# Kernel tuning notes

Measured on AMD Instinct MI355X. Metric: run time of the kernel, lower is better.

## Reference

```python
import jax, jax.numpy as jnp
import numpy as np

# FlowNetC correlation config (kernel_size=1 -> pointwise patch; pad == max_displacement)
PAD = 20
MAX_DISP = 20
STRIDE2 = 2


def setup_inputs() -> dict:
    key = jax.random.key(0)
    k1, k2 = jax.random.split(key)
    B, C, H, W = 4, 256, 96, 96
    input1 = jax.random.normal(k1, (B, C, H, W), dtype=jnp.float32)
    input2 = jax.random.normal(k2, (B, C, H, W), dtype=jnp.float32)
    return {"input1": input1, "input2": input2}


def _correlation(x1, x2):
    # x1, x2: [B, C, H, W]. Output: [B, D*D, H, W] with D = 2*MAX_DISP//STRIDE2 + 1.
    B, C, H, W = x1.shape
    x2p = jnp.pad(x2, ((0, 0), (0, 0), (PAD, PAD), (PAD, PAD)))
    D = 2 * MAX_DISP // STRIDE2 + 1  # 21
    # start index into padded map = PAD + (disp) where disp = off - MAX_DISP;
    # since PAD == MAX_DISP, start index == off.
    offs = jnp.arange(D, dtype=jnp.int32) * STRIDE2
    dyv, dxv = jnp.meshgrid(offs, offs, indexing="ij")
    pairs = jnp.stack([dyv.ravel(), dxv.ravel()], axis=1)  # [D*D, 2]
    inv_c = jnp.float32(1.0 / C)  # CUDA kernel divides by kernel^2 * C (kernel=1)

    def body(_, p):
        dy, dx = p[0], p[1]
        sl = jax.lax.dynamic_slice(x2p, (0, 0, dy, dx), (B, C, H, W))
        return None, jnp.einsum("bchw,bchw->bhw", x1, sl) * inv_c

    _, corr = jax.lax.scan(body, None, pairs)  # [D*D, B, H, W]
    return corr.transpose(1, 0, 2, 3)  # [B, D*D, H, W]


def reference(input1, input2):
    return _correlation(input1, input2)
```

## Files before the change

kernel.cpp:

```cpp
#include <hip/hip_runtime.h>
#include <hip/hip_bf16.h>


typedef __bf16 bf16x8 __attribute__((ext_vector_type(8)));
typedef float f32x4 __attribute__((ext_vector_type(4)));

#define B_ 4
#define C_ 256
#define H_ 96
#define W_ 96
#define NOFF 21
#define ROWS 96
#define IMG_ELEMS (ROWS * C_)
#define HALF_ELEMS (48 * C_)
#define X1T_ELEMS (B_ * H_ * IMG_ELEMS)

__device__ __forceinline__ unsigned short f32_to_bf16_rne(float f) {
    union { float f; unsigned u; } v; v.f = f;
    unsigned u = v.u;
    return (unsigned short)((u + 0x7fffu + ((u >> 16) & 1u)) >> 16);
}

__device__ __forceinline__ void gl2lds16(const void* g, void* l) {
    __builtin_amdgcn_global_load_lds(
        (const __attribute__((address_space(1))) void*)g,
        (__attribute__((address_space(3))) void*)l, 16, 0, 0);
}

__global__ __launch_bounds__(256) void prep_kernel(const float* __restrict__ x1,
                                                   const float* __restrict__ x2,
                                                   unsigned short* __restrict__ ws) {
    __shared__ float tile[96 * 65];
    int bid = blockIdx.x;
    int cblk  = bid & 3;
    int which = (bid >> 2) & 1;
    int bh    = bid >> 3;
    int h = bh % H_;
    int b = bh / H_;
    int c0 = cblk << 6;

    const float* src = (which ? x2 : x1) + ((size_t)(b * C_ + c0) * H_ + h) * W_;
    unsigned short* dst = ws + (size_t)which * X1T_ELEMS + (size_t)(b * H_ + h) * IMG_ELEMS;

    for (int idx = threadIdx.x; idx < 64 * 96; idx += 256) {
        int c = idx / 96, w = idx - c * 96;
        tile[w * 65 + c] = src[c * (H_ * W_) + w];
    }
    __syncthreads();

    for (int idx = threadIdx.x; idx < 96 * 8; idx += 256) {
        int row = idx >> 3, tp = idx & 7;
        int par = row / 48, i = row - par * 48;
        int w = 2 * i + par;
        int s = tp ^ (row & 7);
        const float* fsrc = &tile[w * 65 + (s << 3)];
        unsigned pk[4];
#pragma unroll
        for (int e = 0; e < 4; ++e) {
            unsigned lo = f32_to_bf16_rne(fsrc[2 * e]);
            unsigned hi = f32_to_bf16_rne(fsrc[2 * e + 1]);
            pk[e] = lo | (hi << 16);
        }
        int ccp = (((c0 >> 3) ^ (row & 24)) + tp);
        *(uint4*)((char*)(dst + (size_t)row * C_) + (ccp << 4)) =
            make_uint4(pk[0], pk[1], pk[2], pk[3]);
    }
}

__global__ __launch_bounds__(192, 2) void corr_kernel(const unsigned short* __restrict__ ws,
                                                      float* __restrict__ out) {
    __shared__ unsigned short Bs[2][HALF_ELEMS];
    __shared__ float sl[4][NOFF][49];
    static_assert(sizeof(Bs) + sizeof(sl) <= 81920, "need 2 blocks/CU");

    int bid = blockIdx.x;
    int xcd = bid & 7, sidx = bid >> 3;
    int b  = xcd >> 1;
    int hh = xcd & 1;
    int par = sidx & 1;
    int t2  = sidx >> 1;
    int og  = t2 & 3;
    int qq  = t2 >> 2;
    int gq = qq >> 1, ph = qq & 1;
    int hA = 48 * hh + 8 * gq + ph;
    int olo = (og * NOFF) >> 2;
    int ohi = ((og + 1) * NOFF) >> 2;

    int tid = threadIdx.x;
    int wv = tid >> 6, lane = tid & 63;
    int mt = wv;
    int i0 = mt << 4;
    int n = lane & 15, quad = lane >> 4;

    int Loj[4], Hij[4];
    int tlo = 1 << 30, thi = -(1 << 30);
#pragma unroll
    for (int j = 0; j < 4; ++j) {
        int hj = hA + 2 * j;
        int lo = (hj >= 21) ? 0 : ((21 - hj) >> 1);
        int hi = ((115 - hj) >> 1) + 1;
        if (lo < olo) lo = olo;
        if (hi > ohi) hi = ohi;
        Loj[j] = lo; Hij[j] = hi;
        if (lo < hi) {
            int a = lo + j, c = hi + j;
            if (a < tlo) tlo = a;
            if (c > thi) thi = c;
        }
    }
    int nv = thi - tlo; if (nv < 0) nv = 0;

    int rowA = par * 48 + i0 + n;
    int keyA = rowA & 31;
    bf16x8 af[4][8];
#pragma unroll
    for (int pl = 0; pl < 4; ++pl) {
        const unsigned short* Ag =
            ws + (size_t)(b * H_ + hA + 2 * pl) * IMG_ELEMS + (size_t)rowA * C_;
#pragma unroll
        for (int ks = 0; ks < 8; ++ks)
            af[pl][ks] = *(const bf16x8*)(Ag + ((((ks << 2) | quad) ^ keyA) << 3));
    }
    asm volatile("" ::: "memory");
    __builtin_amdgcn_s_waitcnt(0);

    const unsigned short* Bimg = ws + (size_t)X1T_ELEMS + (size_t)(b * H_) * IMG_ELEMS;

    int wvoff  = wv * 8192;
    int gmaoff = wvoff + lane * 16;

#define STAGE(slot, tt) do {                                                          \
    const char* Bg_ = (const char*)(Bimg + (size_t)(hA + 2 * (tt) - 20) * IMG_ELEMS   \
                                    + par * HALF_ELEMS);                              \
    _Pragma("unroll")                                                                 \
    for (int c = 0; c < 8; ++c)                                                       \
        gl2lds16(Bg_ + gmaoff + c * 1024, (char*)Bs[slot] + wvoff + c * 1024);        \
} while (0)

    if (nv > 0) STAGE(0, tlo);
    if (nv > 1) STAGE(1, tlo + 1);
    asm volatile("" ::: "memory");

#pragma unroll
    for (int pl = 0; pl < 4; ++pl) {
        int hp = hA + 2 * pl;
        for (int oy = olo; oy < ohi; ++oy) {
            if (oy >= Loj[pl] && oy < Hij[pl]) continue;
            int outb = ((b * 441 + oy * NOFF) * H_ + hp) * W_;
#pragma unroll
            for (int jj = 0; jj < 6; ++jj) {
                int idx = tid + jj * 192;
                if (idx < NOFF * 48) {
                    int ox = idx / 48, i = idx - ox * 48;
                    out[outb + ox * (H_ * W_) + 2 * i + par] = 0.0f;
                }
            }
        }
    }

    int locB[3] = { n, n + 16, n + 32 };
    int keyB[3] = { (n + 16 * par) & 31,
                    (n + 16 + 16 * par) & 31,
                    (n + 32 + 16 * par) & 31 };
    bool useu[3] = { mt != 2, true, mt != 0 };

    for (int k = 0; k < nv; ++k) {
        int t = tlo + k;
        int cur = k & 1;

        if (k == 0) {
            if (nv > 1) asm volatile("s_waitcnt vmcnt(8)\ns_barrier" ::: "memory");
            else        asm volatile("s_waitcnt vmcnt(0)\ns_barrier" ::: "memory");
        } else if (k == 1) {
            if (nv > 2) asm volatile("s_waitcnt vmcnt(13)\ns_barrier" ::: "memory");
            else        asm volatile("s_waitcnt vmcnt(5)\ns_barrier" ::: "memory");
        } else if (k + 1 == nv) {
            asm volatile("s_waitcnt vmcnt(10)\ns_barrier" ::: "memory");
        } else {
            asm volatile("s_waitcnt vmcnt(18)\ns_barrier" ::: "memory");
        }

        const char* Bsb = (const char*)Bs[cur];
        f32x4 acc[4][3];
#pragma unroll
        for (int pl = 0; pl < 4; ++pl)
#pragma unroll
            for (int u = 0; u < 3; ++u)
                acc[pl][u] = (f32x4){0.f, 0.f, 0.f, 0.f};

        __builtin_amdgcn_s_setprio(1);
#pragma unroll
        for (int ks = 0; ks < 8; ++ks) {
            int ci = (ks << 2) | quad;
            bf16x8 bfr[3];
#pragma unroll
            for (int u = 0; u < 3; ++u)
                if (useu[u])
                    bfr[u] = *(const bf16x8*)(Bsb + locB[u] * 512 + ((ci ^ keyB[u]) << 4));
#pragma unroll
            for (int u = 0; u < 3; ++u)
                if (useu[u]) {
#pragma unroll
                    for (int pl = 0; pl < 4; ++pl)
                        acc[pl][u] = __builtin_amdgcn_mfma_f32_16x16x32_bf16(
                            af[pl][ks], bfr[u], acc[pl][u], 0, 0, 0);
                }
        }
        __builtin_amdgcn_s_setprio(0);

#pragma unroll
        for (int r = 0; r < 4; ++r) {
            int m = (quad << 2) + r;
            int io = i0 + m;
            int oxb = n - io - 6;
#pragma unroll
            for (int u = 0; u < 3; ++u) {
                if (!useu[u]) continue;
                int ox = 16 * (u + 1) + oxb;
                if (ox >= 0 && ox < NOFF) {
#pragma unroll
                    for (int pl = 0; pl < 4; ++pl)
                        sl[pl][ox][io] = acc[pl][u][r];
                }
            }
        }

        asm volatile("s_waitcnt lgkmcnt(0)\ns_barrier" ::: "memory");

        if (k + 2 < nv) STAGE(cur, t + 2);
        asm volatile("" ::: "memory");

#pragma unroll
        for (int pl = 0; pl < 4; ++pl) {
            int oyp = t - pl;
            if (oyp < Loj[pl] || oyp >= Hij[pl]) continue;
            int hp = hA + 2 * pl;
            int outb = ((b * 441 + oyp * NOFF) * H_ + hp) * W_;
#pragma unroll
            for (int jj = 0; jj < 6; ++jj) {
                int idx = tid + jj * 192;
                if (idx < NOFF * 48) {
                    int ox = idx / 48, i = idx - ox * 48;
                    int w = 2 * i + par;
                    int w2 = w + 2 * ox - 20;
                    float v = (w2 >= 0 && w2 < W_) ? sl[pl][ox][i] * (1.0f / 256.0f) : 0.0f;
                    out[outb + ox * (H_ * W_) + w] = v;
                }
            }
        }
    }
#undef STAGE
}

__global__ __launch_bounds__(256) void corr_fallback(const float* __restrict__ x1,
                                                     const float* __restrict__ x2,
                                                     float* __restrict__ out) {
    int bid = blockIdx.x;
    int oy = bid % NOFF, h = (bid / NOFF) % H_, b = bid / (NOFF * H_);
    int dy = 2 * oy - 20, h2 = h + dy;
    int outbase = ((b * 441 + oy * NOFF) * H_ + h) * W_;
    for (int idx = threadIdx.x; idx < NOFF * W_; idx += 256) {
        int ox = idx / W_, w = idx % W_;
        float acc = 0.f;
        int w2 = w + 2 * ox - 20;
        if (h2 >= 0 && h2 < H_ && w2 >= 0 && w2 < W_) {
            const float* p1 = x1 + (size_t)b * C_ * H_ * W_ + h * W_ + w;
            const float* p2 = x2 + (size_t)b * C_ * H_ * W_ + h2 * W_ + w2;
            for (int c = 0; c < C_; ++c) acc += p1[c * (H_ * W_)] * p2[c * (H_ * W_)];
        }
        out[outbase + ox * (H_ * W_) + w] = acc * (1.0f / 256.0f);
    }
}

extern "C" void kernel_launch(void* const* d_in, const int* in_sizes, int n_in,
                              void* d_out, int out_size, void* d_ws, size_t ws_size,
                              hipStream_t stream) {
    const float* x1 = (const float*)d_in[0];
    const float* x2 = (const float*)d_in[1];
    float* out = (float*)d_out;

    size_t need = (size_t)2 * X1T_ELEMS * sizeof(unsigned short);
    if (ws_size >= need) {
        unsigned short* ws = (unsigned short*)d_ws;
        prep_kernel<<<B_ * H_ * 2 * 4, 256, 0, stream>>>(x1, x2, ws);
        corr_kernel<<<768, 192, 0, stream>>>(ws, out);
    } else {
        corr_fallback<<<B_ * H_ * NOFF, 256, 0, stream>>>(x1, x2, out);
    }
}
```

Baseline: 175.7 us.

## Merge both width parities into one 384-thread block with single-buffered B rows

Each block now holds both column parities (six waves) and three output rows per block instead of four, loading a full 96-row B image into LDS once per displacement rather than separate halves per parity block. Double buffering is dropped in favour of a single LDS buffer staged right after the barrier, and output stores use precomputed per-thread offsets over full 96-wide rows for contiguous writes. Grid shrinks to 512 blocks and targets 3 blocks per CU. The cost is less load/compute overlap and fewer rows sharing each staged B tile.

```diff
diff --git a/kernel.cpp b/kernel.cpp
--- a/kernel.cpp
+++ b/kernel.cpp
@@ -12,7 +12,6 @@
 #define NOFF 21
 #define ROWS 96
 #define IMG_ELEMS (ROWS * C_)
-#define HALF_ELEMS (48 * C_)
 #define X1T_ELEMS (B_ * H_ * IMG_ELEMS)
 
 __device__ __forceinline__ unsigned short f32_to_bf16_rne(float f) {
@@ -67,35 +66,65 @@
     }
 }
 
-__global__ __launch_bounds__(192, 2) void corr_kernel(const unsigned short* __restrict__ ws,
+__global__ __launch_bounds__(384, 3) void corr_kernel(const unsigned short* __restrict__ ws,
                                                       float* __restrict__ out) {
-    __shared__ unsigned short Bs[2][HALF_ELEMS];
-    __shared__ float sl[4][NOFF][49];
+    __shared__ unsigned short Bs[IMG_ELEMS];
+    __shared__ float sl[3][NOFF][97];
     static_assert(sizeof(Bs) + sizeof(sl) <= 81920, "need 2 blocks/CU");
 
     int bid = blockIdx.x;
     int xcd = bid & 7, sidx = bid >> 3;
     int b  = xcd >> 1;
     int hh = xcd & 1;
-    int par = sidx & 1;
-    int t2  = sidx >> 1;
-    int og  = t2 & 3;
-    int qq  = t2 >> 2;
-    int gq = qq >> 1, ph = qq & 1;
-    int hA = 48 * hh + 8 * gq + ph;
+    int og = sidx & 3;
+    int tq = sidx >> 2;
+    int k8 = tq >> 1, ph = tq & 1;
+    int hA = 48 * hh + 6 * k8 + ph;
     int olo = (og * NOFF) >> 2;
     int ohi = ((og + 1) * NOFF) >> 2;
 
     int tid = threadIdx.x;
     int wv = tid >> 6, lane = tid & 63;
-    int mt = wv;
+    int par = wv & 1, mt = wv >> 1;
     int i0 = mt << 4;
     int n = lane & 15, quad = lane >> 4;
 
-    int Loj[4], Hij[4];
+    int jcnt = 5 + (tid < 96 ? 1 : 0);
+    int slotj[6], offj[6]; bool mj[6];
+#pragma unroll
+    for (int j = 0; j < 6; ++j) {
+        int idx = tid + j * 384;
+        int ox = idx / W_, w = idx - ox * W_;
+        slotj[j] = ox * 97 + w;
+        offj[j]  = ox * (H_ * W_) + w;
+        int w2 = w + 2 * ox - 20;
+        mj[j] = (w2 >= 0) & (w2 < W_);
+    }
+
+    int rowA = par * 48 + i0 + n;
+    int keyA = rowA & 31;
+    bf16x8 af[3][8];
+#pragma unroll
+    for (int pl = 0; pl < 3; ++pl) {
+        const unsigned short* Ag =
+            ws + (size_t)(b * H_ + hA + 2 * pl) * IMG_ELEMS + (size_t)rowA * C_;
+#pragma unroll
+        for (int ks = 0; ks < 8; ++ks)
+            af[pl][ks] = *(const bf16x8*)(Ag + ((((ks << 2) | quad) ^ keyA) << 3));
+    }
+    asm volatile("" ::: "memory");
+    __builtin_amdgcn_s_waitcnt(0);
+
+    const unsigned short* Bimg = ws + (size_t)X1T_ELEMS + (size_t)(b * H_) * IMG_ELEMS;
+
+    int rowB[3] = { par * 48 + n, par * 48 + n + 16, par * 48 + n + 32 };
+    int keyB[3] = { rowB[0] & 31, rowB[1] & 31, rowB[2] & 31 };
+    bool useu[3] = { mt != 2, true, mt != 0 };
+
+    int Loj[3], Hij[3];
     int tlo = 1 << 30, thi = -(1 << 30);
 #pragma unroll
-    for (int j = 0; j < 4; ++j) {
+    for (int j = 0; j < 3; ++j) {
         int hj = hA + 2 * j;
         int lo = (hj >= 21) ? 0 : ((21 - hj) >> 1);
         int hi = ((115 - hj) >> 1) + 1;
@@ -103,87 +132,46 @@
         if (hi > ohi) hi = ohi;
         Loj[j] = lo; Hij[j] = hi;
         if (lo < hi) {
-            int a = lo + j, c = hi + j;
-            if (a < tlo) tlo = a;
-            if (c > thi) thi = c;
+            if (lo + j < tlo) tlo = lo + j;
+            if (hi + j > thi) thi = hi + j;
         }
     }
     int nv = thi - tlo; if (nv < 0) nv = 0;
-
-    int rowA = par * 48 + i0 + n;
-    int keyA = rowA & 31;
-    bf16x8 af[4][8];
-#pragma unroll
-    for (int pl = 0; pl < 4; ++pl) {
-        const unsigned short* Ag =
-            ws + (size_t)(b * H_ + hA + 2 * pl) * IMG_ELEMS + (size_t)rowA * C_;
-#pragma unroll
-        for (int ks = 0; ks < 8; ++ks)
-            af[pl][ks] = *(const bf16x8*)(Ag + ((((ks << 2) | quad) ^ keyA) << 3));
-    }
-    asm volatile("" ::: "memory");
-    __builtin_amdgcn_s_waitcnt(0);
-
-    const unsigned short* Bimg = ws + (size_t)X1T_ELEMS + (size_t)(b * H_) * IMG_ELEMS;
 
     int wvoff  = wv * 8192;
     int gmaoff = wvoff + lane * 16;
 
-#define STAGE(slot, tt) do {                                                          \
-    const char* Bg_ = (const char*)(Bimg + (size_t)(hA + 2 * (tt) - 20) * IMG_ELEMS   \
-                                    + par * HALF_ELEMS);                              \
+#define STAGE(tt) do {                                                                \
+    const char* Bg_ = (const char*)(Bimg + (size_t)(hA + 2 * (tt) - 20) * IMG_ELEMS); \
     _Pragma("unroll")                                                                 \
     for (int c = 0; c < 8; ++c)                                                       \
-        gl2lds16(Bg_ + gmaoff + c * 1024, (char*)Bs[slot] + wvoff + c * 1024);        \
+        gl2lds16(Bg_ + gmaoff + c * 1024, (char*)Bs + wvoff + c * 1024);              \
 } while (0)
 
-    if (nv > 0) STAGE(0, tlo);
-    if (nv > 1) STAGE(1, tlo + 1);
+    if (nv > 0) STAGE(tlo);
     asm volatile("" ::: "memory");
 
 #pragma unroll
-    for (int pl = 0; pl < 4; ++pl) {
+    for (int pl = 0; pl < 3; ++pl) {
         int hp = hA + 2 * pl;
         for (int oy = olo; oy < ohi; ++oy) {
             if (oy >= Loj[pl] && oy < Hij[pl]) continue;
             int outb = ((b * 441 + oy * NOFF) * H_ + hp) * W_;
 #pragma unroll
-            for (int jj = 0; jj < 6; ++jj) {
-                int idx = tid + jj * 192;
-                if (idx < NOFF * 48) {
-                    int ox = idx / 48, i = idx - ox * 48;
-                    out[outb + ox * (H_ * W_) + 2 * i + par] = 0.0f;
-                }
-            }
-        }
-    }
-
-    int locB[3] = { n, n + 16, n + 32 };
-    int keyB[3] = { (n + 16 * par) & 31,
-                    (n + 16 + 16 * par) & 31,
-                    (n + 32 + 16 * par) & 31 };
-    bool useu[3] = { mt != 2, true, mt != 0 };
+            for (int j = 0; j < 6; ++j) if (j < jcnt) out[outb + offj[j]] = 0.0f;
+        }
+    }
 
     for (int k = 0; k < nv; ++k) {
         int t = tlo + k;
-        int cur = k & 1;
-
-        if (k == 0) {
-            if (nv > 1) asm volatile("s_waitcnt vmcnt(8)\ns_barrier" ::: "memory");
-            else        asm volatile("s_waitcnt vmcnt(0)\ns_barrier" ::: "memory");
-        } else if (k == 1) {
-            if (nv > 2) asm volatile("s_waitcnt vmcnt(13)\ns_barrier" ::: "memory");
-            else        asm volatile("s_waitcnt vmcnt(5)\ns_barrier" ::: "memory");
-        } else if (k + 1 == nv) {
-            asm volatile("s_waitcnt vmcnt(10)\ns_barrier" ::: "memory");
-        } else {
-            asm volatile("s_waitcnt vmcnt(18)\ns_barrier" ::: "memory");
-        }
-
-        const char* Bsb = (const char*)Bs[cur];
-        f32x4 acc[4][3];
-#pragma unroll
-        for (int pl = 0; pl < 4; ++pl)
+
+        if (k == 0) asm volatile("s_waitcnt vmcnt(0)\ns_barrier" ::: "memory");
+        else        asm volatile("s_waitcnt vmcnt(5)\ns_barrier" ::: "memory");
+
+        const char* Bsb = (const char*)Bs;
+        f32x4 acc[3][3];
+#pragma unroll
+        for (int pl = 0; pl < 3; ++pl)
 #pragma unroll
             for (int u = 0; u < 3; ++u)
                 acc[pl][u] = (f32x4){0.f, 0.f, 0.f, 0.f};
@@ -196,12 +184,12 @@
 #pragma unroll
             for (int u = 0; u < 3; ++u)
                 if (useu[u])
-                    bfr[u] = *(const bf16x8*)(Bsb + locB[u] * 512 + ((ci ^ keyB[u]) << 4));
+                    bfr[u] = *(const bf16x8*)(Bsb + rowB[u] * 512 + ((ci ^ keyB[u]) << 4));
 #pragma unroll
             for (int u = 0; u < 3; ++u)
                 if (useu[u]) {
 #pragma unroll
-                    for (int pl = 0; pl < 4; ++pl)
+                    for (int pl = 0; pl < 3; ++pl)
                         acc[pl][u] = __builtin_amdgcn_mfma_f32_16x16x32_bf16(
                             af[pl][ks], bfr[u], acc[pl][u], 0, 0, 0);
                 }
@@ -211,42 +199,37 @@
 #pragma unroll
         for (int r = 0; r < 4; ++r) {
             int m = (quad << 2) + r;
-            int io = i0 + m;
-            int oxb = n - io - 6;
+            int w = 2 * (i0 + m) + par;
+            int oxb = n - i0 - m - 6;
 #pragma unroll
             for (int u = 0; u < 3; ++u) {
                 if (!useu[u]) continue;
                 int ox = 16 * (u + 1) + oxb;
                 if (ox >= 0 && ox < NOFF) {
 #pragma unroll
-                    for (int pl = 0; pl < 4; ++pl)
-                        sl[pl][ox][io] = acc[pl][u][r];
+                    for (int pl = 0; pl < 3; ++pl) sl[pl][ox][w] = acc[pl][u][r];
                 }
             }
         }
 
         asm volatile("s_waitcnt lgkmcnt(0)\ns_barrier" ::: "memory");
 
-        if (k + 2 < nv) STAGE(cur, t + 2);
+        if (k + 1 < nv) STAGE(t + 1);
         asm volatile("" ::: "memory");
 
 #pragma unroll
-        for (int pl = 0; pl < 4; ++pl) {
+        for (int pl = 0; pl < 3; ++pl) {
             int oyp = t - pl;
             if (oyp < Loj[pl] || oyp >= Hij[pl]) continue;
-            int hp = hA + 2 * pl;
-            int outb = ((b * 441 + oyp * NOFF) * H_ + hp) * W_;
-#pragma unroll
-            for (int jj = 0; jj < 6; ++jj) {
-                int idx = tid + jj * 192;
-                if (idx < NOFF * 48) {
-                    int ox = idx / 48, i = idx - ox * 48;
-                    int w = 2 * i + par;
-                    int w2 = w + 2 * ox - 20;
-                    float v = (w2 >= 0 && w2 < W_) ? sl[pl][ox][i] * (1.0f / 256.0f) : 0.0f;
-                    out[outb + ox * (H_ * W_) + w] = v;
-                }
-            }
+            int outb = ((b * 441 + oyp * NOFF) * H_ + (hA + 2 * pl)) * W_;
+            const float* slp = &sl[pl][0][0];
+            float v[6];
+#pragma unroll
+            for (int j = 0; j < 6; ++j) if (j < jcnt)
+                v[j] = mj[j] ? slp[slotj[j]] * (1.0f / 256.0f) : 0.0f;
+#pragma unroll
+            for (int j = 0; j < 6; ++j) if (j < jcnt)
+                out[outb + offj[j]] = v[j];
         }
     }
 #undef STAGE
@@ -283,7 +266,7 @@
     if (ws_size >= need) {
         unsigned short* ws = (unsigned short*)d_ws;
         prep_kernel<<<B_ * H_ * 2 * 4, 256, 0, stream>>>(x1, x2, ws);
-        corr_kernel<<<768, 192, 0, stream>>>(ws, out);
+        corr_kernel<<<512, 384, 0, stream>>>(ws, out);
     } else {
         corr_fallback<<<B_ * H_ * NOFF, 256, 0, stream>>>(x1, x2, out);
     }
```

Result: slower. 220.4 us (+25.4%).
